# Optimization experiments

Hardware: AMD Instinct MI355X
Metric: run time of the kernel (lower is better)

Reference implementation:

```python
import jax, jax.numpy as jnp
import numpy as np

HIDDEN = 4096
NUM_HEADS = 32
HEAD_DIM = HIDDEN // NUM_HEADS  # 128
ROPE_THETA = 10000.0
B, S = 1, 2048


def setup_inputs() -> dict:
    key = jax.random.key(0)
    k1, k2, k3, k4 = jax.random.split(key, 4)
    positions = jnp.broadcast_to(jnp.arange(S, dtype=jnp.int32), (B, S))
    hidden_states = jax.random.normal(k1, (B, S, HIDDEN), dtype=jnp.float32)
    # fused QKV projection (bias=True), output projection (bias=False)
    w_qkv = jax.random.normal(k2, (HIDDEN, 3 * HIDDEN), dtype=jnp.float32) * (HIDDEN ** -0.5)
    b_qkv = jax.random.normal(k3, (3 * HIDDEN,), dtype=jnp.float32) * 0.01
    w_o = jax.random.normal(k4, (HIDDEN, HIDDEN), dtype=jnp.float32) * (HIDDEN ** -0.5)
    return {"positions": positions, "hidden_states": hidden_states,
            "w_qkv": w_qkv, "b_qkv": b_qkv, "w_o": w_o}


def _apply_rope(x, positions):
    # x: [B, S, N, D]; NeoX-style rotate-half RoPE, rotary_dim == head_dim
    half = HEAD_DIM // 2
    inv_freq = 1.0 / (ROPE_THETA ** (jnp.arange(0, half, dtype=jnp.float32) / half))
    angles = positions.astype(jnp.float32)[..., None] * inv_freq  # [B, S, half]
    cos = jnp.cos(angles)[:, :, None, :]  # [B, S, 1, half]
    sin = jnp.sin(angles)[:, :, None, :]
    x1, x2 = x[..., :half], x[..., half:]
    return jnp.concatenate([x1 * cos - x2 * sin, x2 * cos + x1 * sin], axis=-1)


def reference(positions, hidden_states, w_qkv, b_qkv, w_o):
    qkv = jnp.einsum('bsh,hd->bsd', hidden_states, w_qkv) + b_qkv  # [B, S, 3H]
    q, k, v = jnp.split(qkv, 3, axis=-1)
    q = q.reshape(B, S, NUM_HEADS, HEAD_DIM)
    k = k.reshape(B, S, NUM_HEADS, HEAD_DIM)
    v = v.reshape(B, S, NUM_HEADS, HEAD_DIM)
    q = _apply_rope(q, positions)
    k = _apply_rope(k, positions)
    scale = HEAD_DIM ** -0.5
    scores = jnp.einsum('bqnd,bknd->bnqk', q, k) * scale  # [B, N, S, S]
    causal = jnp.tril(jnp.ones((S, S), dtype=bool))
    scores = jnp.where(causal, scores, jnp.finfo(scores.dtype).min)
    probs = jax.nn.softmax(scores, axis=-1)
    attn = jnp.einsum('bnqk,bknd->bqnd', probs, v).reshape(B, S, HIDDEN)
    return jnp.einsum('bsh,ho->bso', attn, w_o)
```

## Files before the change

kernel.cpp:

```cpp
#include <hip/hip_runtime.h>
#include <hip/hip_bf16.h>

#define S_LEN 2048
#define HID   4096
#define NH    32
#define HD    128
#define KD    4096

typedef __attribute__((ext_vector_type(4))) float f32x4;
typedef __attribute__((ext_vector_type(8))) short s16x8;
typedef __attribute__((ext_vector_type(4))) short s16x4;

#define AS1 __attribute__((address_space(1)))
#define AS3 __attribute__((address_space(3)))

__device__ __forceinline__ void gl_lds16(const void* g, void* l) {
  __builtin_amdgcn_global_load_lds((const AS1 void*)g, (AS3 void*)l, 16, 0, 0);
}

__device__ inline short f2bf(float f) {
  union { float f; unsigned u; } v; v.f = f;
  return (short)((v.u + 0x7fffu + ((v.u >> 16) & 1u)) >> 16);
}
__device__ inline float bf2f(short s) {
  union { unsigned u; float f; } v; v.u = ((unsigned)(unsigned short)s) << 16;
  return v.f;
}
__device__ inline unsigned packbf(float a, float b) {
  return (unsigned)(unsigned short)f2bf(a) | ((unsigned)(unsigned short)f2bf(b) << 16);
}

__global__ __launch_bounds__(256)
void cvt_kernel(const float* __restrict__ A, short* __restrict__ Ab) {
  const size_t i = ((size_t)blockIdx.x * 256 + threadIdx.x) * 8;
  f32x4 v0 = *(const f32x4*)&A[i];
  f32x4 v1 = *(const f32x4*)&A[i + 4];
  s16x8 r;
  r[0]=f2bf(v0[0]); r[1]=f2bf(v0[1]); r[2]=f2bf(v0[2]); r[3]=f2bf(v0[3]);
  r[4]=f2bf(v1[0]); r[5]=f2bf(v1[1]); r[6]=f2bf(v1[2]); r[7]=f2bf(v1[3]);
  *(s16x8*)&Ab[i] = r;
}

__global__ __launch_bounds__(256)
void transcvt_kernel(const float* __restrict__ W, short* __restrict__ Wt, const int N) {
  __shared__ float tile[64][65];
  const int k0 = blockIdx.x * 64, n0 = blockIdx.y * 64;
  const int t = threadIdx.x;
#pragma unroll
  for (int i = 0; i < 16; ++i) {
    const int e = i * 256 + t;
    const int k = e >> 6, n = e & 63;
    tile[n][k] = W[(size_t)(k0 + k) * N + n0 + n];
  }
  __syncthreads();
  const int nn = t >> 2, ks = (t & 3) * 16;
  s16x8 a, b;
#pragma unroll
  for (int i = 0; i < 8; i++) a[i] = f2bf(tile[nn][ks + i]);
#pragma unroll
  for (int i = 0; i < 8; i++) b[i] = f2bf(tile[nn][ks + 8 + i]);
  *(s16x8*)&Wt[(size_t)(n0 + nn) * KD + k0 + ks]     = a;
  *(s16x8*)&Wt[(size_t)(n0 + nn) * KD + k0 + ks + 8] = b;
}

template<int EPI>
__global__ __launch_bounds__(256, 2)
void gemm5_kernel(const short* __restrict__ A, const short* __restrict__ Bt,
                  const float* __restrict__ bias,
                  short* __restrict__ Qb, short* __restrict__ Kb, short* __restrict__ Vb,
                  float* __restrict__ Cout)
{
  __shared__ char sm[3][24576] __attribute__((aligned(128)));
  const int KD2 = KD * 2;
  const int bid = blockIdx.x;
  const int xcd = bid & 7, idx = bid >> 3;
  const int m0 = (idx & 7) * 256;
  const int n0 = (xcd * ((EPI == 0) ? 12 : 4) + (idx >> 3)) * 128;

  const int t = threadIdx.x, lane = t & 63, c = lane & 15, g = lane >> 4;
  const int w = t >> 6, wr = w >> 1, wc = w & 1;
  const int flip = ((c >> 1) & 7) << 4;
  const int laneA = wr * 8192 + ((c * 64 + g * 16) ^ flip);
  const int laneB = 16384 + wc * 4096 + ((c * 64 + g * 16) ^ flip);

  const char* srcA[4];
  const char* srcB[2];
#pragma unroll
  for (int j = 0; j < 4; ++j) {
    const int la = j * 4096 + t * 16;
    const int ls = la ^ ((la >> 3) & 0x70);
    srcA[j] = (const char*)A + (size_t)(m0 + (ls >> 6)) * KD2 + (ls & 63);
  }
#pragma unroll
  for (int j = 0; j < 2; ++j) {
    const int la = j * 4096 + t * 16;
    const int ls = la ^ ((la >> 3) & 0x70);
    srcB[j] = (const char*)Bt + (size_t)(n0 + (ls >> 6)) * KD2 + (ls & 63);
  }

  f32x4 acc[8][4];
#pragma unroll
  for (int i = 0; i < 8; i++)
#pragma unroll
    for (int j = 0; j < 4; j++) acc[i][j] = (f32x4){0.f, 0.f, 0.f, 0.f};

#define STG(S, H) do {                                        \
    const size_t ko_ = (size_t)(H) * 64;                      \
    gl_lds16(srcA[0] + ko_, sm[S] + t * 16);                  \
    gl_lds16(srcA[1] + ko_, sm[S] + 4096  + t * 16);          \
    gl_lds16(srcA[2] + ko_, sm[S] + 8192  + t * 16);          \
    gl_lds16(srcA[3] + ko_, sm[S] + 12288 + t * 16);          \
    gl_lds16(srcB[0] + ko_, sm[S] + 16384 + t * 16);          \
    gl_lds16(srcB[1] + ko_, sm[S] + 20480 + t * 16);          \
  } while (0)

#define COMP(S) do {                                                       \
    const char* b_ = sm[S];                                                \
    s16x8 a_[8], bb_[4];                                                   \
    _Pragma("unroll")                                                      \
    for (int mi = 0; mi < 8; ++mi) a_[mi] = *(const s16x8*)(b_ + laneA + mi * 1024); \
    _Pragma("unroll")                                                      \
    for (int ni = 0; ni < 4; ++ni) bb_[ni] = *(const s16x8*)(b_ + laneB + ni * 1024); \
    __builtin_amdgcn_s_setprio(1);                                         \
    _Pragma("unroll")                                                      \
    for (int mi = 0; mi < 8; ++mi)                                         \
      _Pragma("unroll")                                                    \
      for (int ni = 0; ni < 4; ++ni)                                       \
        acc[mi][ni] = __builtin_amdgcn_mfma_f32_16x16x32_bf16(a_[mi], bb_[ni], acc[mi][ni], 0, 0, 0); \
    __builtin_amdgcn_s_setprio(0);                                         \
  } while (0)

#define WAIT6 asm volatile("s_waitcnt vmcnt(6)" ::: "memory")
#define WAIT0 asm volatile("s_waitcnt vmcnt(0)" ::: "memory")
#define BARR  do { __builtin_amdgcn_s_barrier(); asm volatile("" ::: "memory"); } while (0)

  STG(0, 0); STG(1, 1);
  for (int j = 0; j < 42; ++j) {
    const int h = 3 * j;
    WAIT6; BARR; STG(2, h + 2); COMP(0);
    WAIT6; BARR; STG(0, h + 3); COMP(1);
    WAIT6; BARR; STG(1, h + 4); COMP(2);
  }
  WAIT6; BARR; COMP(0);
  WAIT0; BARR; COMP(1);

#undef STG
#undef COMP
#undef WAIT6
#undef WAIT0
#undef BARR

  if (EPI == 0) {
#pragma unroll
    for (int ni = 0; ni < 4; ++ni) {
      const int ncol = n0 + wc * 64 + ni * 16 + c;
      const int which = ncol >> 12;
      const int h = (ncol >> 7) & 31;
      const int dcl = ncol & 127;
      short* dst = (which == 0) ? Qb : ((which == 1) ? Kb : Vb);
      const float bv = bias[ncol];
#pragma unroll
      for (int mi = 0; mi < 8; ++mi)
#pragma unroll
        for (int jj = 0; jj < 4; ++jj) {
          const int row = m0 + wr * 128 + mi * 16 + g * 4 + jj;
          dst[((size_t)h * S_LEN + row) * HD + dcl] = f2bf(acc[mi][ni][jj] + bv);
        }
    }
  } else {
#pragma unroll
    for (int ni = 0; ni < 4; ++ni) {
      const int ncol = n0 + wc * 64 + ni * 16 + c;
#pragma unroll
      for (int mi = 0; mi < 8; ++mi)
#pragma unroll
        for (int jj = 0; jj < 4; ++jj) {
          const int row = m0 + wr * 128 + mi * 16 + g * 4 + jj;
          Cout[(size_t)row * HID + ncol] = acc[mi][ni][jj];
        }
    }
  }
}

template<int EPI, int ABF16>
__global__ __launch_bounds__(256)
void gemm_kernel(const void* __restrict__ Av, const float* __restrict__ B,
                 const float* __restrict__ bias, const int N,
                 short* __restrict__ Qb, short* __restrict__ Kb, short* __restrict__ Vb,
                 float* __restrict__ Cout)
{
  __shared__ short As[128][40];
  __shared__ short Bs[128][40];
  const int m0 = blockIdx.x * 128;
  const int nb = blockIdx.y * 128;
  const int t  = threadIdx.x;
  const int w = t >> 6, lane = t & 63, c = lane & 15, g = lane >> 4;
  const int wm = (w >> 1) * 64, wn = (w & 1) * 64;

  f32x4 acc[4][4];
#pragma unroll
  for (int i = 0; i < 4; i++)
#pragma unroll
    for (int j = 0; j < 4; j++) acc[i][j] = (f32x4){0.f, 0.f, 0.f, 0.f};

  const int ar = t >> 3;
  const int ac = (t & 7) * 4;
  const int bn = t & 127;
  const int bkq = (t >> 7) * 16;

  for (int k0 = 0; k0 < KD; k0 += 32) {
#pragma unroll
    for (int rr = 0; rr < 4; rr++) {
      const int row = rr * 32 + ar;
      if (ABF16) {
        *(s16x4*)&As[row][ac] =
          *(const s16x4*)((const short*)Av + (size_t)(m0 + row) * KD + k0 + ac);
      } else {
        f32x4 v = *(const f32x4*)((const float*)Av + (size_t)(m0 + row) * KD + k0 + ac);
        s16x4 pk;
        pk[0] = f2bf(v[0]); pk[1] = f2bf(v[1]); pk[2] = f2bf(v[2]); pk[3] = f2bf(v[3]);
        *(s16x4*)&As[row][ac] = pk;
      }
    }
    const float* pB = B + (size_t)(k0 + bkq) * N + nb + bn;
    s16x8 b0, b1;
#pragma unroll
    for (int i = 0; i < 8; i++) b0[i] = f2bf(pB[(size_t)i * N]);
#pragma unroll
    for (int i = 0; i < 8; i++) b1[i] = f2bf(pB[(size_t)(i + 8) * N]);
    *(s16x8*)&Bs[bn][bkq]     = b0;
    *(s16x8*)&Bs[bn][bkq + 8] = b1;
    __syncthreads();
    s16x8 af[4], bfr[4];
#pragma unroll
    for (int i = 0; i < 4; i++) af[i]  = *(const s16x8*)&As[wm + i * 16 + c][g * 8];
#pragma unroll
    for (int i = 0; i < 4; i++) bfr[i] = *(const s16x8*)&Bs[wn + i * 16 + c][g * 8];
#pragma unroll
    for (int mi = 0; mi < 4; mi++)
#pragma unroll
      for (int ni = 0; ni < 4; ni++)
        acc[mi][ni] = __builtin_amdgcn_mfma_f32_16x16x32_bf16(af[mi], bfr[ni], acc[mi][ni], 0, 0, 0);
    __syncthreads();
  }

  if (EPI == 0) {
    const int which = nb >> 12;
    const int h = (nb & 4095) >> 7;
    short* dst = (which == 0) ? Qb : ((which == 1) ? Kb : Vb);
#pragma unroll
    for (int ni = 0; ni < 4; ni++) {
      const int d = wn + ni * 16 + c;
      const float bv = bias[nb + d];
#pragma unroll
      for (int mi = 0; mi < 4; mi++)
#pragma unroll
        for (int j = 0; j < 4; j++) {
          const int row = m0 + wm + mi * 16 + g * 4 + j;
          dst[((size_t)h * S_LEN + row) * HD + d] = f2bf(acc[mi][ni][j] + bv);
        }
    }
  } else {
#pragma unroll
    for (int ni = 0; ni < 4; ni++) {
      const int n = nb + wn + ni * 16 + c;
#pragma unroll
      for (int mi = 0; mi < 4; mi++)
#pragma unroll
        for (int j = 0; j < 4; j++) {
          const int row = m0 + wm + mi * 16 + g * 4 + j;
          Cout[(size_t)row * N + n] = acc[mi][ni][j];
        }
    }
  }
}

__global__ void rope_kernel(const int* __restrict__ positions,
                            short* __restrict__ Qb, short* __restrict__ Kb)
{
  const int s = blockIdx.x;
  const int h = blockIdx.y * 4 + threadIdx.y;
  const int d = threadIdx.x;
  const float pos = (float)positions[s];
  const float inv_freq = exp2f(-(float)d * 0.20762050593046014f);
  const float ang = pos * inv_freq;
  float sn, cs;
  sincosf(ang, &sn, &cs);
  const size_t base = ((size_t)h * S_LEN + s) * HD + d;
  const float scale = 0.08838834764831845f;
  float x1 = bf2f(Qb[base]), x2 = bf2f(Qb[base + 64]);
  Qb[base]      = f2bf((x1 * cs - x2 * sn) * scale);
  Qb[base + 64] = f2bf((x2 * cs + x1 * sn) * scale);
  x1 = bf2f(Kb[base]); x2 = bf2f(Kb[base + 64]);
  Kb[base]      = f2bf(x1 * cs - x2 * sn);
  Kb[base + 64] = f2bf(x2 * cs + x1 * sn);
}

__global__ __launch_bounds__(256)
void vtrans_kernel(const short* __restrict__ V, short* __restrict__ Vt)
{
  __shared__ short tile[64][72];
  const int h = blockIdx.z;
  const int s0 = blockIdx.x * 64;
  const int d0 = blockIdx.y * 64;
  const int tx = threadIdx.x & 63, ty = threadIdx.x >> 6;
  for (int r = ty; r < 64; r += 4)
    tile[r][tx] = V[((size_t)h * S_LEN + s0 + r) * HD + d0 + tx];
  __syncthreads();
  for (int r = ty; r < 64; r += 4)
    Vt[((size_t)h * HD + d0 + r) * S_LEN + s0 + tx] = tile[tx][r];
}

__global__ __launch_bounds__(512)
void attn_kernel(const short* __restrict__ Q, const short* __restrict__ Kg,
                 const short* __restrict__ Vtg, short* __restrict__ attn_out)
{
  __shared__ short Ks[2][64][128];
  __shared__ short Vs[2][128][72];
  const int h = blockIdx.y;
  const int q0 = blockIdx.x * 128;
  const int t = threadIdx.x;
  const int w = t >> 6, lane = t & 63, c = lane & 15, g = lane >> 4;
  const short* Qh = Q   + (size_t)h * S_LEN * HD;
  const short* Kh = Kg  + (size_t)h * S_LEN * HD;
  const short* Vh = Vtg + (size_t)h * HD * S_LEN;

  const int krow = t >> 4, kch = t & 15;
  const int vrow = t >> 3, vch = t & 7;
  const int ksw = (kch ^ ((krow & 3) | ((krow >> 1) & 4))) * 16;

  const int rbase = (c >> 2) * 8 + (c & 3);
  const int sb = (rbase & 3) | ((rbase >> 1) & 4);
  int koff[4];
#pragma unroll
  for (int di = 0; di < 4; ++di) koff[di] = ((di * 4 + g) ^ sb) * 16;

  const int qg = q0 + w * 16 + c;
  s16x8 qf[4];
#pragma unroll
  for (int di = 0; di < 4; di++)
    qf[di] = *(const s16x8*)&Qh[(size_t)qg * HD + di * 32 + g * 8];

  f32x4 o[8];
#pragma unroll
  for (int dt = 0; dt < 8; dt++) o[dt] = (f32x4){0.f, 0.f, 0.f, 0.f};
  float m_r = -3.0e38f, l_r = 0.f;

  const int nt = q0 / 64 + 2;

  {
#pragma unroll
    for (int i = 0; i < 2; ++i) {
      s16x8 gK = *(const s16x8*)&Kh[(size_t)(i * 32 + krow) * HD + kch * 8];
      s16x8 gV = *(const s16x8*)&Vh[(size_t)(i * 64 + vrow) * S_LEN + vch * 8];
      *(s16x8*)((char*)&Ks[0][0][0] + (i * 32 + krow) * 256 + ksw) = gK;
      *(s16x8*)&Vs[0][i * 64 + vrow][vch * 8] = gV;
    }
  }
  __syncthreads();

  for (int kt = 0; kt < nt; kt++) {
    const int cur = kt & 1;
    const int kb = kt * 64;
    s16x8 gK0, gK1, gV0, gV1;
    if (kt + 1 < nt) {
      gK0 = *(const s16x8*)&Kh[(size_t)(kb + 64 + krow) * HD + kch * 8];
      gK1 = *(const s16x8*)&Kh[(size_t)(kb + 96 + krow) * HD + kch * 8];
      gV0 = *(const s16x8*)&Vh[(size_t)vrow * S_LEN + kb + 64 + vch * 8];
      gV1 = *(const s16x8*)&Vh[(size_t)(64 + vrow) * S_LEN + kb + 64 + vch * 8];
    }
    f32x4 sA = (f32x4){0,0,0,0}, sB = (f32x4){0,0,0,0};
    f32x4 sC = (f32x4){0,0,0,0}, sD = (f32x4){0,0,0,0};
    const char* kb_ = (const char*)&Ks[cur][0][0] + rbase * 256;
#pragma unroll
    for (int di = 0; di < 4; ++di) {
      const char* p = kb_ + koff[di];
      s16x8 kA = *(const s16x8*)(p);
      s16x8 kB = *(const s16x8*)(p + 1024);
      s16x8 kC = *(const s16x8*)(p + 8192);
      s16x8 kD = *(const s16x8*)(p + 9216);
      sA = __builtin_amdgcn_mfma_f32_16x16x32_bf16(kA, qf[di], sA, 0, 0, 0);
      sB = __builtin_amdgcn_mfma_f32_16x16x32_bf16(kB, qf[di], sB, 0, 0, 0);
      sC = __builtin_amdgcn_mfma_f32_16x16x32_bf16(kC, qf[di], sC, 0, 0, 0);
      sD = __builtin_amdgcn_mfma_f32_16x16x32_bf16(kD, qf[di], sD, 0, 0, 0);
    }
    float v[16];
#pragma unroll
    for (int j = 0; j < 4; ++j) {
      v[j]      = (kb + 8 * g + j      <= qg) ? sA[j] : -__builtin_inff();
      v[4 + j]  = (kb + 8 * g + 4 + j  <= qg) ? sB[j] : -__builtin_inff();
      v[8 + j]  = (kb + 32 + 8 * g + j     <= qg) ? sC[j] : -__builtin_inff();
      v[12 + j] = (kb + 32 + 8 * g + 4 + j <= qg) ? sD[j] : -__builtin_inff();
    }
    float mx = v[0];
#pragma unroll
    for (int i = 1; i < 16; ++i) mx = fmaxf(mx, v[i]);
    mx = fmaxf(mx, __shfl_xor(mx, 16, 64));
    mx = fmaxf(mx, __shfl_xor(mx, 32, 64));
    const float mn = fmaxf(m_r, mx);
    if (!__all(mn - m_r <= 8.0f)) {
      const float al = __expf(m_r - mn);
      l_r *= al;
#pragma unroll
      for (int dt = 0; dt < 8; dt++)
#pragma unroll
        for (int j = 0; j < 4; j++) o[dt][j] *= al;
      m_r = mn;
    }
    float p[16];
    float rs = 0.f;
#pragma unroll
    for (int i = 0; i < 16; ++i) { p[i] = __expf(v[i] - m_r); rs += p[i]; }
    rs += __shfl_xor(rs, 16, 64);
    rs += __shfl_xor(rs, 32, 64);
    l_r += rs;
    union { s16x8 v8; unsigned u[4]; } pb0, pb1;
    pb0.u[0] = packbf(p[0], p[1]);   pb0.u[1] = packbf(p[2], p[3]);
    pb0.u[2] = packbf(p[4], p[5]);   pb0.u[3] = packbf(p[6], p[7]);
    pb1.u[0] = packbf(p[8], p[9]);   pb1.u[1] = packbf(p[10], p[11]);
    pb1.u[2] = packbf(p[12], p[13]); pb1.u[3] = packbf(p[14], p[15]);
#pragma unroll
    for (int dt = 0; dt < 8; dt++) {
      s16x8 vf0 = *(const s16x8*)&Vs[cur][dt * 16 + c][g * 8];
      s16x8 vf1 = *(const s16x8*)&Vs[cur][dt * 16 + c][32 + g * 8];
      o[dt] = __builtin_amdgcn_mfma_f32_16x16x32_bf16(vf0, pb0.v8, o[dt], 0, 0, 0);
      o[dt] = __builtin_amdgcn_mfma_f32_16x16x32_bf16(vf1, pb1.v8, o[dt], 0, 0, 0);
    }
    __syncthreads();
    if (kt + 1 < nt) {
      *(s16x8*)((char*)&Ks[cur ^ 1][0][0] + krow * 256 + ksw)        = gK0;
      *(s16x8*)((char*)&Ks[cur ^ 1][0][0] + (32 + krow) * 256 + ksw) = gK1;
      *(s16x8*)&Vs[cur ^ 1][vrow][vch * 8]      = gV0;
      *(s16x8*)&Vs[cur ^ 1][64 + vrow][vch * 8] = gV1;
    }
    __syncthreads();
  }

  const float inv_l = 1.0f / l_r;
#pragma unroll
  for (int dt = 0; dt < 8; dt++) {
    s16x4 pk;
#pragma unroll
    for (int j = 0; j < 4; j++) pk[j] = f2bf(o[dt][j] * inv_l);
    *(s16x4*)&attn_out[(size_t)qg * HID + h * HD + dt * 16 + g * 4] = pk;
  }
}

extern "C" void kernel_launch(void* const* d_in, const int* in_sizes, int n_in,
                              void* d_out, int out_size, void* d_ws, size_t ws_size,
                              hipStream_t stream)
{
  const int*   positions = (const int*)d_in[0];
  const float* hidden    = (const float*)d_in[1];
  const float* w_qkv     = (const float*)d_in[2];
  const float* b_qkv     = (const float*)d_in[3];
  const float* w_o       = (const float*)d_in[4];
  float* out = (float*)d_out;

  char* ws = (char*)d_ws;
  const size_t MB = (size_t)1 << 20;

  if (ws_size >= 224 * MB) {
    short* Ah    = (short*)(ws);
    short* Wqt   = (short*)(ws + 16 * MB);
    short* Wot   = (short*)(ws + 112 * MB);
    short* Qb    = (short*)(ws + 144 * MB);
    short* Kb    = (short*)(ws + 160 * MB);
    short* Vb    = (short*)(ws + 176 * MB);
    short* Vt    = (short*)(ws + 192 * MB);
    short* attnb = (short*)(ws + 208 * MB);

    cvt_kernel<<<4096, 256, 0, stream>>>(hidden, Ah);
    transcvt_kernel<<<dim3(KD / 64, 3 * HID / 64), 256, 0, stream>>>(w_qkv, Wqt, 3 * HID);
    transcvt_kernel<<<dim3(KD / 64, HID / 64), 256, 0, stream>>>(w_o, Wot, HID);
    gemm5_kernel<0><<<768, 256, 0, stream>>>(Ah, Wqt, b_qkv, Qb, Kb, Vb, nullptr);
    rope_kernel<<<dim3(S_LEN, NH / 4), dim3(64, 4), 0, stream>>>(positions, Qb, Kb);
    vtrans_kernel<<<dim3(S_LEN / 64, HD / 64, NH), 256, 0, stream>>>(Vb, Vt);
    attn_kernel<<<dim3(S_LEN / 128, NH), 512, 0, stream>>>(Qb, Kb, Vt, attnb);
    gemm5_kernel<1><<<256, 256, 0, stream>>>(attnb, Wot, nullptr,
                                             nullptr, nullptr, nullptr, out);
  } else {
    short* Qb    = (short*)(ws);
    short* Kb    = (short*)(ws + 16 * MB);
    short* Vb    = (short*)(ws + 32 * MB);
    short* Vt    = (short*)(ws + 48 * MB);
    short* attnb = (short*)(ws + 64 * MB);

    gemm_kernel<0, 0><<<dim3(16, 96), 256, 0, stream>>>(hidden, w_qkv, b_qkv, 3 * HID,
                                                        Qb, Kb, Vb, nullptr);
    rope_kernel<<<dim3(S_LEN, NH / 4), dim3(64, 4), 0, stream>>>(positions, Qb, Kb);
    vtrans_kernel<<<dim3(S_LEN / 64, HD / 64, NH), 256, 0, stream>>>(Vb, Vt);
    attn_kernel<<<dim3(S_LEN / 128, NH), 512, 0, stream>>>(Qb, Kb, Vt, attnb);
    gemm_kernel<1, 1><<<dim3(16, 32), 256, 0, stream>>>(attnb, w_o, nullptr, HID,
                                                        nullptr, nullptr, nullptr, out);
  }
}
```

Baseline: 485.3 us.

## Add 128x128-tile triple-buffered GEMM for output projection with XCD-aware block mapping

Replaces the output-projection GEMM (previously gemm5 with 256 blocks) with a new gemm7 kernel using 128x128 tiles, 512 blocks, three LDS stages fed by global_load_lds with swizzled addresses, and a block-to-tile mapping that groups N tiles per XCD. The aim is to fill all CUs with more blocks and overlap loads with MFMA compute better, while improving L2 locality per XCD. Smaller tiles mean more reloading of A/B from memory, and the hardcoded loop count assumes K=4096.

New measurement: 495.5 us. 2.1% more time.

```diff
diff --git a/kernel.cpp b/kernel.cpp
--- a/kernel.cpp
+++ b/kernel.cpp
@@ -179,6 +179,96 @@
           Cout[(size_t)row * HID + ncol] = acc[mi][ni][jj];
         }
     }
+  }
+}
+
+__global__ __launch_bounds__(256, 3)
+void gemm7_kernel(const short* __restrict__ A, const short* __restrict__ Bt,
+                  float* __restrict__ Cout)
+{
+  __shared__ char sm[3][16384] __attribute__((aligned(128)));
+  const int KD2 = KD * 2;
+  const int bid = blockIdx.x;
+  const int xcd = bid & 7, idx = bid >> 3;
+  const int m0 = (idx & 15) * 128;
+  const int n0 = (xcd * 4 + (idx >> 4)) * 128;
+
+  const int t = threadIdx.x, lane = t & 63, c = lane & 15, g = lane >> 4;
+  const int w = t >> 6, wr = w >> 1, wc = w & 1;
+  const int flip = ((c >> 1) & 7) << 4;
+  const int laneA = wr * 4096 + ((c * 64 + g * 16) ^ flip);
+  const int laneB = 8192 + wc * 4096 + ((c * 64 + g * 16) ^ flip);
+
+  const char* srcA[2];
+  const char* srcB[2];
+#pragma unroll
+  for (int j = 0; j < 2; ++j) {
+    const int la = j * 4096 + t * 16;
+    const int ls = la ^ ((la >> 3) & 0x70);
+    srcA[j] = (const char*)A  + (size_t)(m0 + (ls >> 6)) * KD2 + (ls & 63);
+    srcB[j] = (const char*)Bt + (size_t)(n0 + (ls >> 6)) * KD2 + (ls & 63);
+  }
+
+  f32x4 acc[4][4];
+#pragma unroll
+  for (int i = 0; i < 4; i++)
+#pragma unroll
+    for (int j = 0; j < 4; j++) acc[i][j] = (f32x4){0.f, 0.f, 0.f, 0.f};
+
+#define STG7(S, H) do {                                       \
+    const size_t ko_ = (size_t)(H) * 64;                      \
+    gl_lds16(srcA[0] + ko_, sm[S] + t * 16);                  \
+    gl_lds16(srcA[1] + ko_, sm[S] + 4096  + t * 16);          \
+    gl_lds16(srcB[0] + ko_, sm[S] + 8192  + t * 16);          \
+    gl_lds16(srcB[1] + ko_, sm[S] + 12288 + t * 16);          \
+  } while (0)
+
+#define COMP7(S) do {                                                      \
+    const char* b_ = sm[S];                                                \
+    s16x8 a_[4], bb_[4];                                                   \
+    _Pragma("unroll")                                                      \
+    for (int mi = 0; mi < 4; ++mi) a_[mi] = *(const s16x8*)(b_ + laneA + mi * 1024); \
+    _Pragma("unroll")                                                      \
+    for (int ni = 0; ni < 4; ++ni) bb_[ni] = *(const s16x8*)(b_ + laneB + ni * 1024); \
+    __builtin_amdgcn_s_setprio(1);                                         \
+    _Pragma("unroll")                                                      \
+    for (int mi = 0; mi < 4; ++mi)                                         \
+      _Pragma("unroll")                                                    \
+      for (int ni = 0; ni < 4; ++ni)                                       \
+        acc[mi][ni] = __builtin_amdgcn_mfma_f32_16x16x32_bf16(a_[mi], bb_[ni], acc[mi][ni], 0, 0, 0); \
+    __builtin_amdgcn_s_setprio(0);                                         \
+  } while (0)
+
+#define WAIT4 asm volatile("s_waitcnt vmcnt(4)" ::: "memory")
+#define WAIT0 asm volatile("s_waitcnt vmcnt(0)" ::: "memory")
+#define BARR  do { __builtin_amdgcn_s_barrier(); asm volatile("" ::: "memory"); } while (0)
+
+  STG7(0, 0); STG7(1, 1);
+  for (int j = 0; j < 42; ++j) {
+    const int h = 3 * j;
+    WAIT4; BARR; STG7(2, h + 2); COMP7(0);
+    WAIT4; BARR; STG7(0, h + 3); COMP7(1);
+    WAIT4; BARR; STG7(1, h + 4); COMP7(2);
+  }
+  WAIT4; BARR; COMP7(0);
+  WAIT0; BARR; COMP7(1);
+
+#undef STG7
+#undef COMP7
+#undef WAIT4
+#undef WAIT0
+#undef BARR
+
+#pragma unroll
+  for (int ni = 0; ni < 4; ++ni) {
+    const int ncol = n0 + wc * 64 + ni * 16 + c;
+#pragma unroll
+    for (int mi = 0; mi < 4; ++mi)
+#pragma unroll
+      for (int jj = 0; jj < 4; ++jj) {
+        const int row = m0 + wr * 64 + mi * 16 + g * 4 + jj;
+        Cout[(size_t)row * HID + ncol] = acc[mi][ni][jj];
+      }
   }
 }
 
@@ -477,8 +567,7 @@
     rope_kernel<<<dim3(S_LEN, NH / 4), dim3(64, 4), 0, stream>>>(positions, Qb, Kb);
     vtrans_kernel<<<dim3(S_LEN / 64, HD / 64, NH), 256, 0, stream>>>(Vb, Vt);
     attn_kernel<<<dim3(S_LEN / 128, NH), 512, 0, stream>>>(Qb, Kb, Vt, attnb);
-    gemm5_kernel<1><<<256, 256, 0, stream>>>(attnb, Wot, nullptr,
-                                             nullptr, nullptr, nullptr, out);
+    gemm7_kernel<<<512, 256, 0, stream>>>(attnb, Wot, out);
   } else {
     short* Qb    = (short*)(ws);
     short* Kb    = (short*)(ws + 16 * MB);
```
